# Kernel optimization log

Measured on AMD Instinct MI355X. Metric: run time of the kernel, lower is better.

The kernel has to match this reference:

```python
import jax, jax.numpy as jnp
import numpy as np

NUM_HEADS = 16
NEG_BIG = 1e9


def setup_inputs() -> dict:
    key = jax.random.key(0)
    k1, k2, k3 = jax.random.split(key, 3)
    B, T, D = 2, 2048, 1024
    x = jax.random.normal(k1, (B, T, D), dtype=jnp.float32)
    W_attn = jax.random.normal(k2, (D, 3 * D), dtype=jnp.float32) * 0.02
    b_attn = jnp.zeros((3 * D,), dtype=jnp.float32)
    W_proj = jax.random.normal(k3, (D, D), dtype=jnp.float32) * 0.02
    b_proj = jnp.zeros((D,), dtype=jnp.float32)
    return {"x": x, "W_attn": W_attn, "b_attn": b_attn, "W_proj": W_proj, "b_proj": b_proj}


def reference(x, W_attn, b_attn, W_proj, b_proj):
    B, T, D = x.shape
    H = NUM_HEADS
    dh = D // H
    # qkv projection (GPT-style Conv1D == linear)
    qkv = jnp.einsum('btd,de->bte', x, W_attn) + b_attn  # [B,T,3D]
    q, k, v = jnp.split(qkv, 3, axis=-1)
    # split heads -> [B,H,T,dh]
    q = q.reshape(B, T, H, dh).transpose(0, 2, 1, 3)
    k = k.reshape(B, T, H, dh).transpose(0, 2, 1, 3)
    v = v.reshape(B, T, H, dh).transpose(0, 2, 1, 3)
    # scores [B,H,T,T]; scale=True divides by sqrt(head_dim)
    w = jnp.einsum('bhqd,bhkd->bhqk', q, k) / jnp.sqrt(jnp.float32(dh))
    # causal mask: multiplicative tril then large additive negative, as in source
    mask = jnp.tril(jnp.ones((T, T), dtype=w.dtype))[None, None, :, :]
    w = w * mask - NEG_BIG * (1.0 - mask)
    p = jax.nn.softmax(w, axis=-1)  # attn dropout = identity (eval mode)
    out = jnp.einsum('bhqk,bhkd->bhqd', p, v)  # [B,H,T,dh]
    out = out.transpose(0, 2, 1, 3).reshape(B, T, D)  # merge heads
    out = jnp.einsum('btd,de->bte', out, W_proj) + b_proj  # residual dropout = identity
    return out
```

## Files before the change

### kernel.cpp

```cpp
#include <hip/hip_runtime.h>

typedef unsigned short u16;
typedef unsigned u32;
typedef __bf16 bf16x8 __attribute__((ext_vector_type(8)));
typedef __bf16 bf16x2 __attribute__((ext_vector_type(2)));
typedef float f32x4 __attribute__((ext_vector_type(4)));
typedef u16 u16x4 __attribute__((ext_vector_type(4)));
typedef u32 u32x2 __attribute__((ext_vector_type(2)));
typedef u32 u32x4 __attribute__((ext_vector_type(4)));

__device__ __forceinline__ u16 f2bf(float f) {
  u32 u = __float_as_uint(f);
  u += 0x7fffu + ((u >> 16) & 1u);
  return (u16)(u >> 16);
}

__device__ __forceinline__ u32 pk2(float a, float b) {
#if __has_builtin(__builtin_amdgcn_cvt_pk_bf16_f32)
  bf16x2 r = __builtin_amdgcn_cvt_pk_bf16_f32(a, b);
  return __builtin_bit_cast(u32, r);
#else
  return (u32)f2bf(a) | ((u32)f2bf(b) << 16);
#endif
}

__device__ __forceinline__ float fast_exp2(float x) {
  return __builtin_amdgcn_exp2f(x);
}

__device__ __forceinline__ void gload16(const u16* g, u16* l) {
  __builtin_amdgcn_global_load_lds((__attribute__((address_space(1))) void*)g,
                                   (__attribute__((address_space(3))) void*)l,
                                   16, 0, 0);
}

__global__ __launch_bounds__(256) void prep(const float* __restrict__ x,
                                            u16* __restrict__ xb,
                                            const float* __restrict__ Wa,
                                            u16* __restrict__ wat,
                                            const float* __restrict__ Wp,
                                            u16* __restrict__ wpt) {
  __shared__ float tile[32][33];
  const int bid = blockIdx.x;
  if (bid < 4096) {
    int i = bid * 256 + threadIdx.x;
    float4 v = ((const float4*)x)[i];
    u16x4 o = { f2bf(v.x), f2bf(v.y), f2bf(v.z), f2bf(v.w) };
    ((u16x4*)xb)[i] = o;
    return;
  }
  const float* in; u16* out; int C, bx, by;
  if (bid < 7168) { int id = bid - 4096; bx = id % 96; by = id / 96; in = Wa; out = wat; C = 3072; }
  else            { int id = bid - 7168; bx = id & 31; by = id >> 5; in = Wp; out = wpt; C = 1024; }
  const int R = 1024;
  int c0 = bx * 32, r0 = by * 32;
  int tx = threadIdx.x & 31, ty = threadIdx.x >> 5;
#pragma unroll
  for (int i = 0; i < 32; i += 8)
    tile[ty + i][tx] = in[(size_t)(r0 + ty + i) * C + c0 + tx];
  __syncthreads();
#pragma unroll
  for (int i = 0; i < 32; i += 8)
    out[(size_t)(c0 + ty + i) * R + r0 + tx] = f2bf(tile[tx][ty + i]);
}

template <int EPI>
__global__ __launch_bounds__(256) void gemm_bt(const u16* __restrict__ A,
                                               const u16* __restrict__ Bt, int K,
                                               const float* __restrict__ bias,
                                               float* __restrict__ outF,
                                               u16* __restrict__ qb, u16* __restrict__ kb,
                                               u16* __restrict__ vtb) {
  __shared__ __align__(16) u16 As[128 * 32];
  __shared__ __align__(16) u16 Bs[128 * 32];
  const int tid = threadIdx.x;
  const int w = tid >> 6, lane = tid & 63, quad = lane >> 4, l16 = lane & 15;
  const int wm = w >> 1, wn = w & 1;
  const int tm = blockIdx.y * 128, tn = blockIdx.x * 128;

  f32x4 acc[4][4] = {};

  const int ra = lane >> 2;
  const int ca = (lane & 3) * 8;
  const u16* gA0 = A + (size_t)(tm + w * 16 + ra) * K + ca;
  const u16* gA1 = A + (size_t)(tm + (w + 4) * 16 + ra) * K + ca;
  const u16* gB0 = Bt + (size_t)(tn + w * 16 + ra) * K + ca;
  const u16* gB1 = Bt + (size_t)(tn + (w + 4) * 16 + ra) * K + ca;
  u16* lA0 = &As[(w * 16) * 32];
  u16* lA1 = &As[((w + 4) * 16) * 32];
  u16* lB0 = &Bs[(w * 16) * 32];
  u16* lB1 = &Bs[((w + 4) * 16) * 32];

  for (int k0 = 0; k0 < K; k0 += 32) {
    gload16(gA0 + k0, lA0);
    gload16(gA1 + k0, lA1);
    gload16(gB0 + k0, lB0);
    gload16(gB1 + k0, lB1);
    __syncthreads();
    bf16x8 af[4], bfr[4];
#pragma unroll
    for (int mt = 0; mt < 4; ++mt)
      af[mt] = *(const bf16x8*)&As[(wm * 64 + mt * 16 + l16) * 32 + quad * 8];
#pragma unroll
    for (int nt = 0; nt < 4; ++nt)
      bfr[nt] = *(const bf16x8*)&Bs[(wn * 64 + nt * 16 + l16) * 32 + quad * 8];
#pragma unroll
    for (int mt = 0; mt < 4; ++mt)
#pragma unroll
      for (int nt = 0; nt < 4; ++nt)
        acc[mt][nt] = __builtin_amdgcn_mfma_f32_16x16x32_bf16(af[mt], bfr[nt], acc[mt][nt], 0, 0, 0);
    __syncthreads();
  }

#pragma unroll
  for (int mt = 0; mt < 4; ++mt) {
#pragma unroll
    for (int nt = 0; nt < 4; ++nt) {
      const int row0 = tm + wm * 64 + mt * 16 + quad * 4;
      const int col = tn + wn * 64 + nt * 16 + l16;
      float v4[4];
#pragma unroll
      for (int r = 0; r < 4; ++r) v4[r] = acc[mt][nt][r] + bias[col];
      if (EPI == 0) {
        int which = col >> 10, d = col & 1023, hh = d >> 6, dd = d & 63;
        int b = row0 >> 11, t = row0 & 2047;
        int bh = (b << 4) + hh;
        if (which == 0) {
#pragma unroll
          for (int r = 0; r < 4; ++r)
            qb[((size_t)bh * 2048 + t + r) * 64 + dd] = f2bf(v4[r] * 0.18033688f);
        } else if (which == 1) {
#pragma unroll
          for (int r = 0; r < 4; ++r)
            kb[((size_t)bh * 2048 + t + r) * 64 + dd] = f2bf(v4[r]);
        } else {
          u16x4 pk = { f2bf(v4[0]), f2bf(v4[1]), f2bf(v4[2]), f2bf(v4[3]) };
          *(u16x4*)(vtb + ((size_t)bh * 64 + dd) * 2048 + t) = pk;
        }
      } else {
#pragma unroll
        for (int r = 0; r < 4; ++r)
          outF[(size_t)(row0 + r) * 1024 + col] = v4[r];
      }
    }
  }
}

__global__ __launch_bounds__(256) void gemm_p64(const u16* __restrict__ A,
                                                const u16* __restrict__ Bt,
                                                const float* __restrict__ bias,
                                                float* __restrict__ outF) {
  const int K = 1024;
  __shared__ __align__(16) u16 As[64 * 32];
  __shared__ __align__(16) u16 Bs[64 * 32];
  const int tid = threadIdx.x;
  const int w = tid >> 6, lane = tid & 63, quad = lane >> 4, l16 = lane & 15;
  const int tm = blockIdx.y * 64, tn = blockIdx.x * 64;

  f32x4 acc[4] = {};

  const int ra = tid >> 2;
  const int ca = (tid & 3) * 8;
  const u16* gA0 = A + (size_t)(tm + ra) * K + ca;
  const u16* gB0 = Bt + (size_t)(tn + ra) * K + ca;
  u16* lA0 = &As[(w * 16) * 32];
  u16* lB0 = &Bs[(w * 16) * 32];

  for (int k0 = 0; k0 < K; k0 += 32) {
    gload16(gA0 + k0, lA0);
    gload16(gB0 + k0, lB0);
    __syncthreads();
    bf16x8 bf = *(const bf16x8*)&Bs[(w * 16 + l16) * 32 + quad * 8];
#pragma unroll
    for (int mt = 0; mt < 4; ++mt) {
      bf16x8 af = *(const bf16x8*)&As[(mt * 16 + l16) * 32 + quad * 8];
      acc[mt] = __builtin_amdgcn_mfma_f32_16x16x32_bf16(af, bf, acc[mt], 0, 0, 0);
    }
    __syncthreads();
  }

#pragma unroll
  for (int mt = 0; mt < 4; ++mt) {
    const int row0 = tm + mt * 16 + quad * 4;
    const int col = tn + w * 16 + l16;
#pragma unroll
    for (int r = 0; r < 4; ++r)
      outF[(size_t)(row0 + r) * 1024 + col] = acc[mt][r] + bias[col];
  }
}

__global__ __launch_bounds__(256) void flash_attn(const u16* __restrict__ qb,
                                                  const u16* __restrict__ kb,
                                                  const u16* __restrict__ vtb,
                                                  u16* __restrict__ ao) {
  const int T = 2048;
  const int tid = threadIdx.x;
  const int w = tid >> 6, lane = tid & 63;
  const int quad = lane >> 4, l16 = lane & 15;
  const int bx = blockIdx.x;
  const int bh = bx & 31;
  const int g0 = bx >> 5;
  const int G = (g0 & 24) | (((g0 >> 3) & 1) ? (7 - (g0 & 7)) : (g0 & 7));
  const int b = bh >> 4, h = bh & 15;
  const int ro = w * 16 + l16;
  const int qrow = G * 64 + ro;
  const size_t kvbase = (size_t)bh * T * 64;
  const int nkt = G + 1;

  __shared__ __align__(16) u16 Ks[64][72];
  __shared__ __align__(16) u16 Vs[64][72];
  __shared__ __align__(16) u16 Ps[4][16][72];

  bf16x8 q0 = *(const bf16x8*)(qb + kvbase + (size_t)qrow * 64 + quad * 8);
  bf16x8 q1 = *(const bf16x8*)(qb + kvbase + (size_t)qrow * 64 + 32 + quad * 8);

  bf16x8 ones;
#pragma unroll
  for (int i = 0; i < 8; ++i) ones[i] = (__bf16)1.0f;

  f32x4 o[4] = {};
  f32x4 o_lp = {};

  const int tok = tid >> 2, c4 = (tid & 3) * 16;
  const u16* kg = kb + kvbase + (size_t)tok * 64 + c4;
  const u16* vg = vtb + (size_t)(bh * 64 + tok) * 2048 + c4;

  {
    u32x4 a0 = *(const u32x4*)(kg);
    u32x4 a1 = *(const u32x4*)(kg + 8);
    u32x4 b0 = *(const u32x4*)(vg);
    u32x4 b1 = *(const u32x4*)(vg + 8);
    *(u32x4*)&Ks[tok][c4] = a0;  *(u32x4*)&Ks[tok][c4 + 8] = a1;
    *(u32x4*)&Vs[tok][c4] = b0;  *(u32x4*)&Vs[tok][c4 + 8] = b1;
  }
  __syncthreads();

  u32x4 sk0, sk1, sv0, sv1;

  for (int kt = 0; kt < nkt; ++kt) {
    const bool more = (kt + 1 < nkt);
    if (more) {
      const int kb2 = (kt + 1) * 64;
      sk0 = *(const u32x4*)(kg + (size_t)kb2 * 64);
      sk1 = *(const u32x4*)(kg + (size_t)kb2 * 64 + 8);
      sv0 = *(const u32x4*)(vg + kb2);
      sv1 = *(const u32x4*)(vg + kb2 + 8);
    }

    f32x4 z[4];
#pragma unroll
    for (int st = 0; st < 4; ++st) {
      bf16x8 kf0 = *(const bf16x8*)&Ks[st * 16 + l16][quad * 8];
      bf16x8 kf1 = *(const bf16x8*)&Ks[st * 16 + l16][32 + quad * 8];
      f32x4 zz = {};
      zz = __builtin_amdgcn_mfma_f32_16x16x32_bf16(kf0, q0, zz, 0, 0, 0);
      zz = __builtin_amdgcn_mfma_f32_16x16x32_bf16(kf1, q1, zz, 0, 0, 0);
      z[st] = zz;
    }
    if (kt == nkt - 1) {
#pragma unroll
      for (int st = 0; st < 4; ++st)
#pragma unroll
        for (int r = 0; r < 4; ++r)
          if (st * 16 + quad * 4 + r > ro) z[st][r] = -1e30f;
    }
#pragma unroll
    for (int st = 0; st < 4; ++st) {
      float p0 = fast_exp2(z[st][0]), p1 = fast_exp2(z[st][1]);
      float p2 = fast_exp2(z[st][2]), p3 = fast_exp2(z[st][3]);
      u32x2 pw = { pk2(p0, p1), pk2(p2, p3) };
      *(u32x2*)&Ps[w][l16][st * 16 + quad * 4] = pw;
    }

    bf16x8 pf0 = *(const bf16x8*)&Ps[w][l16][quad * 8];
    bf16x8 pf1 = *(const bf16x8*)&Ps[w][l16][32 + quad * 8];
    o_lp = __builtin_amdgcn_mfma_f32_16x16x32_bf16(ones, pf0, o_lp, 0, 0, 0);
    o_lp = __builtin_amdgcn_mfma_f32_16x16x32_bf16(ones, pf1, o_lp, 0, 0, 0);
#pragma unroll
    for (int dt = 0; dt < 4; ++dt) {
      bf16x8 vf0 = *(const bf16x8*)&Vs[dt * 16 + l16][quad * 8];
      bf16x8 vf1 = *(const bf16x8*)&Vs[dt * 16 + l16][32 + quad * 8];
      o[dt] = __builtin_amdgcn_mfma_f32_16x16x32_bf16(vf0, pf0, o[dt], 0, 0, 0);
      o[dt] = __builtin_amdgcn_mfma_f32_16x16x32_bf16(vf1, pf1, o[dt], 0, 0, 0);
    }

    __syncthreads();
    if (more) {
      *(u32x4*)&Ks[tok][c4] = sk0;  *(u32x4*)&Ks[tok][c4 + 8] = sk1;
      *(u32x4*)&Vs[tok][c4] = sv0;  *(u32x4*)&Vs[tok][c4 + 8] = sv1;
    }
    __syncthreads();
  }

  float inv = 1.0f / o_lp[0];
  size_t obase = ((size_t)b * T + qrow) * 1024 + h * 64;
#pragma unroll
  for (int dt = 0; dt < 4; ++dt) {
    u16x4 ov = { f2bf(o[dt][0] * inv), f2bf(o[dt][1] * inv),
                 f2bf(o[dt][2] * inv), f2bf(o[dt][3] * inv) };
    *(u16x4*)(ao + obase + dt * 16 + quad * 4) = ov;
  }
}

extern "C" void kernel_launch(void* const* d_in, const int* in_sizes, int n_in,
                              void* d_out, int out_size, void* d_ws, size_t ws_size,
                              hipStream_t stream) {
  const float* x      = (const float*)d_in[0];
  const float* W_attn = (const float*)d_in[1];
  const float* b_attn = (const float*)d_in[2];
  const float* W_proj = (const float*)d_in[3];
  const float* b_proj = (const float*)d_in[4];
  float* out = (float*)d_out;

  if (ws_size < 50331648u) return;

  char* ws = (char*)d_ws;
  u16* xb  = (u16*)(ws);
  u16* wat = (u16*)(ws + 8388608u);
  u16* wpt = (u16*)(ws + 14680064u);
  u16* qb  = (u16*)(ws + 16777216u);
  u16* kb  = (u16*)(ws + 25165824u);
  u16* vtb = (u16*)(ws + 33554432u);
  u16* ao  = (u16*)(ws + 41943040u);

  prep<<<8192, 256, 0, stream>>>(x, xb, W_attn, wat, W_proj, wpt);

  gemm_bt<0><<<dim3(24, 32), 256, 0, stream>>>(xb, wat, 1024, b_attn, nullptr, qb, kb, vtb);

  flash_attn<<<dim3(1024), 256, 0, stream>>>(qb, kb, vtb, ao);

  gemm_p64<<<dim3(16, 64), 256, 0, stream>>>(ao, wpt, b_proj, out);
}
```

Before: 182.6 us.

## Pair complementary causal query tiles in one block to share K/V tiles

```diff
diff --git a/kernel.cpp b/kernel.cpp
--- a/kernel.cpp
+++ b/kernel.cpp
@@ -189,7 +189,7 @@
   }
 }
 
-__global__ __launch_bounds__(256) void flash_attn(const u16* __restrict__ qb,
+__global__ __launch_bounds__(512) void flash_attn(const u16* __restrict__ qb,
                                                   const u16* __restrict__ kb,
                                                   const u16* __restrict__ vtb,
                                                   u16* __restrict__ ao) {
@@ -199,17 +199,19 @@
   const int quad = lane >> 4, l16 = lane & 15;
   const int bx = blockIdx.x;
   const int bh = bx & 31;
-  const int g0 = bx >> 5;
-  const int G = (g0 & 24) | (((g0 >> 3) & 1) ? (7 - (g0 & 7)) : (g0 & 7));
+  const int g = bx >> 5;
+  const int t2 = 31 - g;
   const int b = bh >> 4, h = bh & 15;
-  const int ro = w * 16 + l16;
-  const int qrow = G * 64 + ro;
+  const int grp = w >> 2;
+  const int myt = grp ? t2 : g;
+  const int ro = (w & 3) * 16 + l16;
+  const int qrow = myt * 64 + ro;
   const size_t kvbase = (size_t)bh * T * 64;
-  const int nkt = G + 1;
+  const int nkt = t2 + 1;
 
   __shared__ __align__(16) u16 Ks[64][72];
   __shared__ __align__(16) u16 Vs[64][72];
-  __shared__ __align__(16) u16 Ps[4][16][72];
+  __shared__ __align__(16) u16 Ps[8][16][72];
 
   bf16x8 q0 = *(const bf16x8*)(qb + kvbase + (size_t)qrow * 64 + quad * 8);
   bf16x8 q1 = *(const bf16x8*)(qb + kvbase + (size_t)qrow * 64 + 32 + quad * 8);
@@ -221,73 +223,72 @@
   f32x4 o[4] = {};
   f32x4 o_lp = {};
 
-  const int tok = tid >> 2, c4 = (tid & 3) * 16;
-  const u16* kg = kb + kvbase + (size_t)tok * 64 + c4;
-  const u16* vg = vtb + (size_t)(bh * 64 + tok) * 2048 + c4;
+  const int tok = tid >> 3, c8 = (tid & 7) * 8;
+  const u16* kg = kb + kvbase + (size_t)tok * 64 + c8;
+  const u16* vg = vtb + (size_t)(bh * 64 + tok) * 2048 + c8;
 
   {
     u32x4 a0 = *(const u32x4*)(kg);
-    u32x4 a1 = *(const u32x4*)(kg + 8);
     u32x4 b0 = *(const u32x4*)(vg);
-    u32x4 b1 = *(const u32x4*)(vg + 8);
-    *(u32x4*)&Ks[tok][c4] = a0;  *(u32x4*)&Ks[tok][c4 + 8] = a1;
-    *(u32x4*)&Vs[tok][c4] = b0;  *(u32x4*)&Vs[tok][c4 + 8] = b1;
+    *(u32x4*)&Ks[tok][c8] = a0;
+    *(u32x4*)&Vs[tok][c8] = b0;
   }
   __syncthreads();
 
-  u32x4 sk0, sk1, sv0, sv1;
+  u32x4 sk0, sv0;
 
   for (int kt = 0; kt < nkt; ++kt) {
     const bool more = (kt + 1 < nkt);
     if (more) {
       const int kb2 = (kt + 1) * 64;
       sk0 = *(const u32x4*)(kg + (size_t)kb2 * 64);
-      sk1 = *(const u32x4*)(kg + (size_t)kb2 * 64 + 8);
       sv0 = *(const u32x4*)(vg + kb2);
-      sv1 = *(const u32x4*)(vg + kb2 + 8);
-    }
-
-    f32x4 z[4];
-#pragma unroll
-    for (int st = 0; st < 4; ++st) {
-      bf16x8 kf0 = *(const bf16x8*)&Ks[st * 16 + l16][quad * 8];
-      bf16x8 kf1 = *(const bf16x8*)&Ks[st * 16 + l16][32 + quad * 8];
-      f32x4 zz = {};
-      zz = __builtin_amdgcn_mfma_f32_16x16x32_bf16(kf0, q0, zz, 0, 0, 0);
-      zz = __builtin_amdgcn_mfma_f32_16x16x32_bf16(kf1, q1, zz, 0, 0, 0);
-      z[st] = zz;
-    }
-    if (kt == nkt - 1) {
-#pragma unroll
-      for (int st = 0; st < 4; ++st)
-#pragma unroll
-        for (int r = 0; r < 4; ++r)
-          if (st * 16 + quad * 4 + r > ro) z[st][r] = -1e30f;
-    }
-#pragma unroll
-    for (int st = 0; st < 4; ++st) {
-      float p0 = fast_exp2(z[st][0]), p1 = fast_exp2(z[st][1]);
-      float p2 = fast_exp2(z[st][2]), p3 = fast_exp2(z[st][3]);
-      u32x2 pw = { pk2(p0, p1), pk2(p2, p3) };
-      *(u32x2*)&Ps[w][l16][st * 16 + quad * 4] = pw;
-    }
-
-    bf16x8 pf0 = *(const bf16x8*)&Ps[w][l16][quad * 8];
-    bf16x8 pf1 = *(const bf16x8*)&Ps[w][l16][32 + quad * 8];
-    o_lp = __builtin_amdgcn_mfma_f32_16x16x32_bf16(ones, pf0, o_lp, 0, 0, 0);
-    o_lp = __builtin_amdgcn_mfma_f32_16x16x32_bf16(ones, pf1, o_lp, 0, 0, 0);
-#pragma unroll
-    for (int dt = 0; dt < 4; ++dt) {
-      bf16x8 vf0 = *(const bf16x8*)&Vs[dt * 16 + l16][quad * 8];
-      bf16x8 vf1 = *(const bf16x8*)&Vs[dt * 16 + l16][32 + quad * 8];
-      o[dt] = __builtin_amdgcn_mfma_f32_16x16x32_bf16(vf0, pf0, o[dt], 0, 0, 0);
-      o[dt] = __builtin_amdgcn_mfma_f32_16x16x32_bf16(vf1, pf1, o[dt], 0, 0, 0);
+    }
+
+    const bool act = grp ? true : (kt <= g);
+    if (act) {
+      f32x4 z[4];
+#pragma unroll
+      for (int st = 0; st < 4; ++st) {
+        bf16x8 kf0 = *(const bf16x8*)&Ks[st * 16 + l16][quad * 8];
+        bf16x8 kf1 = *(const bf16x8*)&Ks[st * 16 + l16][32 + quad * 8];
+        f32x4 zz = {};
+        zz = __builtin_amdgcn_mfma_f32_16x16x32_bf16(kf0, q0, zz, 0, 0, 0);
+        zz = __builtin_amdgcn_mfma_f32_16x16x32_bf16(kf1, q1, zz, 0, 0, 0);
+        z[st] = zz;
+      }
+      if (kt == myt) {
+#pragma unroll
+        for (int st = 0; st < 4; ++st)
+#pragma unroll
+          for (int r = 0; r < 4; ++r)
+            if (st * 16 + quad * 4 + r > ro) z[st][r] = -1e30f;
+      }
+#pragma unroll
+      for (int st = 0; st < 4; ++st) {
+        float p0 = fast_exp2(z[st][0]), p1 = fast_exp2(z[st][1]);
+        float p2 = fast_exp2(z[st][2]), p3 = fast_exp2(z[st][3]);
+        u32x2 pw = { pk2(p0, p1), pk2(p2, p3) };
+        *(u32x2*)&Ps[w][l16][st * 16 + quad * 4] = pw;
+      }
+
+      bf16x8 pf0 = *(const bf16x8*)&Ps[w][l16][quad * 8];
+      bf16x8 pf1 = *(const bf16x8*)&Ps[w][l16][32 + quad * 8];
+      o_lp = __builtin_amdgcn_mfma_f32_16x16x32_bf16(ones, pf0, o_lp, 0, 0, 0);
+      o_lp = __builtin_amdgcn_mfma_f32_16x16x32_bf16(ones, pf1, o_lp, 0, 0, 0);
+#pragma unroll
+      for (int dt = 0; dt < 4; ++dt) {
+        bf16x8 vf0 = *(const bf16x8*)&Vs[dt * 16 + l16][quad * 8];
+        bf16x8 vf1 = *(const bf16x8*)&Vs[dt * 16 + l16][32 + quad * 8];
+        o[dt] = __builtin_amdgcn_mfma_f32_16x16x32_bf16(vf0, pf0, o[dt], 0, 0, 0);
+        o[dt] = __builtin_amdgcn_mfma_f32_16x16x32_bf16(vf1, pf1, o[dt], 0, 0, 0);
+      }
     }
 
     __syncthreads();
     if (more) {
-      *(u32x4*)&Ks[tok][c4] = sk0;  *(u32x4*)&Ks[tok][c4 + 8] = sk1;
-      *(u32x4*)&Vs[tok][c4] = sv0;  *(u32x4*)&Vs[tok][c4 + 8] = sv1;
+      *(u32x4*)&Ks[tok][c8] = sk0;
+      *(u32x4*)&Vs[tok][c8] = sv0;
     }
     __syncthreads();
   }
@@ -327,7 +328,7 @@
 
   gemm_bt<0><<<dim3(24, 32), 256, 0, stream>>>(xb, wat, 1024, b_attn, nullptr, qb, kb, vtb);
 
-  flash_attn<<<dim3(1024), 256, 0, stream>>>(qb, kb, vtb, ao);
+  flash_attn<<<dim3(512), 512, 0, stream>>>(qb, kb, vtb, ao);
 
   gemm_p64<<<dim3(16, 64), 256, 0, stream>>>(ao, wpt, b_proj, out);
 }
```

New measurement: 183.7 us. No clear change (+0.6%).
